# Performance work log

Measured on AMD Instinct MI355X. Metric: run time of the kernel, lower is better.

## Reference

```python
import jax, jax.numpy as jnp
import numpy as np

HEAD = 8
DIM_IN = 512
PAD = (4, 4)            # pad = head - dim % head = 8 -> (4, 4)
DIM = DIM_IN + sum(PAD) # 520
DH = DIM // HEAD        # 65


def setup_inputs() -> dict:
    key = jax.random.key(0)
    k1, k2, k3, k4 = jax.random.split(key, 4)
    B, L = 4, 2048
    inp = jax.random.normal(k1, (B, L, DIM_IN), dtype=jnp.float32)
    # nn.Linear weights, shape (out, in), bias=False
    scale = 1.0 / np.sqrt(DIM)
    w_q = jax.random.uniform(k2, (DIM, DIM), jnp.float32, -scale, scale)
    w_k = jax.random.uniform(k3, (DIM, DIM), jnp.float32, -scale, scale)
    w_v = jax.random.uniform(k4, (DIM, DIM), jnp.float32, -scale, scale)
    return {"inp": inp, "w_q": w_q, "w_k": w_k, "w_v": w_v}


def reference(inp, w_q, w_k, w_v):
    # F.pad(inp, pad) pads the last (feature) dim
    x = jnp.pad(inp, ((0, 0), (0, 0), (PAD[0], PAD[1])))
    B, L, D = x.shape
    # project then split heads: [B, H, L, dh]
    def proj(w):
        return (x @ w.T).reshape(B, L, HEAD, DH).transpose(0, 2, 1, 3)
    q, k, v = proj(w_q), proj(w_k), proj(w_v)
    score = jnp.einsum('bhqd,bhkd->bhqk', q, k) / jnp.sqrt(jnp.float32(DH))
    attn = jax.nn.softmax(score, axis=-1)          # [B, H, L, L]
    # dropout is identity in eval/reference mode
    out = jnp.einsum('bhqk,bhkd->bhqd', attn, v)
    out = out.transpose(0, 2, 1, 3).reshape(B, L, D)
    out = out[:, :, PAD[0]:-PAD[1]]                # strip feature padding
    return out, attn
```

## Files before the change

### kernel.cpp

```cpp
#include <hip/hip_runtime.h>

typedef unsigned short u16;
typedef __bf16 bf16x8 __attribute__((ext_vector_type(8)));
typedef float f32x16 __attribute__((ext_vector_type(16)));
typedef unsigned short ushort8 __attribute__((ext_vector_type(8)));

#define LOG2E 1.44269504088896340736f
#define QSCALE 0.12403473458920846f

__device__ __forceinline__ u16 f2bf(float f) {
  unsigned u = __float_as_uint(f);
  u = (u + 0x7fffu + ((u >> 16) & 1u)) >> 16;
  return (u16)u;
}

__device__ __forceinline__ f32x16 zero16() {
  f32x16 z;
#pragma unroll
  for (int i = 0; i < 16; ++i) z[i] = 0.0f;
  return z;
}

__device__ __forceinline__ void gload_lds16(const u16* g, u16* l) {
  __builtin_amdgcn_global_load_lds(
      (const __attribute__((address_space(1))) void*)g,
      (__attribute__((address_space(3))) void*)l, 16, 0, 0);
}

__global__ __launch_bounds__(256) void cvt_x_kernel(const float4* __restrict__ in,
                                                    ushort4* __restrict__ out) {
  int i = blockIdx.x * 256 + threadIdx.x;
  float4 v = in[i];
  ushort4 o;
  o.x = f2bf(v.x); o.y = f2bf(v.y); o.z = f2bf(v.z); o.w = f2bf(v.w);
  out[i] = o;
}

__global__ __launch_bounds__(256) void cvt_w_kernel(const float* __restrict__ wq,
                                                    const float* __restrict__ wk,
                                                    const float* __restrict__ wv,
                                                    u16* __restrict__ wtt) {
  int id = blockIdx.x * 256 + threadIdx.x;
  int wsel = id / (544 * 512);
  int rem = id - wsel * (544 * 512);
  int j = rem >> 9, k = rem & 511;
  const float* wp = (wsel == 0) ? wq : (wsel == 1) ? wk : wv;
  float v = (j < 520) ? wp[j * 520 + k + 4] : 0.0f;
  wtt[id] = f2bf(v);
}

__global__ __launch_bounds__(256) void zero_kernel(uint4* __restrict__ p, int n) {
  int i = blockIdx.x * 256 + threadIdx.x;
  uint4 z = make_uint4(0u, 0u, 0u, 0u);
  for (; i < n; i += gridDim.x * 256) p[i] = z;
}

__global__ __launch_bounds__(256) void proj_kernel(const u16* __restrict__ xb,
                                                   const u16* __restrict__ wtt,
                                                   u16* __restrict__ qb,
                                                   u16* __restrict__ kpl,
                                                   u16* __restrict__ vb) {
  int tid = threadIdx.x;
  int w = tid >> 6, l = tid & 63, lr = l & 31, lh = l >> 5;
  int m0 = blockIdx.y * 128 + w * 32;
  int g = blockIdx.x;

  const u16* ap = xb + (size_t)(m0 + lr) * 512 + lh * 8;

  f32x16 acc[4];
  const u16* bp[4];
  bool valid[4];
#pragma unroll
  for (int i = 0; i < 4; ++i) {
    int nt = g * 4 + i;
    valid[i] = (nt < 51);
    int ntc = valid[i] ? nt : 50;
    bp[i] = wtt + ((size_t)((ntc / 17) * 544 + (ntc % 17) * 32) + lr) * 512 + lh * 8;
    acc[i] = zero16();
  }

#pragma unroll 4
  for (int s = 0; s < 32; ++s) {
    bf16x8 a = *reinterpret_cast<const bf16x8*>(ap + s * 16);
#pragma unroll
    for (int i = 0; i < 4; ++i) {
      if (valid[i]) {
        bf16x8 b = *reinterpret_cast<const bf16x8*>(bp[i] + s * 16);
        acc[i] = __builtin_amdgcn_mfma_f32_32x32x16_bf16(a, b, acc[i], 0, 0, 0);
      }
    }
  }

#pragma unroll
  for (int i = 0; i < 4; ++i) {
    int nt = g * 4 + i;
    if (nt < 51) {
      int wsel = nt / 17;
      int j = (nt % 17) * 32 + lr;
      if (j < 520) {
        int h = j / 65, dh = j - h * 65;
#pragma unroll
        for (int r = 0; r < 16; ++r) {
          int m = m0 + (r & 3) + 8 * (r >> 2) + 4 * lh;
          int bb = m >> 11, lrow = m & 2047;
          int bh = bb * 8 + h;
          if (wsel == 0) {
            qb[((size_t)bh * 2048 + lrow) * 80 + dh] = f2bf(acc[i][r] * QSCALE);
          } else if (wsel == 1) {
            kpl[(((size_t)bh * 10 + (dh >> 3)) * 2048 + lrow) * 8 + (dh & 7)] = f2bf(acc[i][r]);
          } else {
            vb[((size_t)bh * 2048 + lrow) * 80 + dh] = f2bf(acc[i][r]);
          }
        }
      }
    }
  }
}

__global__ __launch_bounds__(256) void repack_v_kernel(const u16* __restrict__ vb,
                                                       u16* __restrict__ vpl) {
  __shared__ u16 lds[256 * 88];
  int bh = blockIdx.y;
  int key0 = blockIdx.x * 256;
  int t = threadIdx.x;

  const u16* src = vb + ((size_t)bh * 2048 + key0) * 80;
#pragma unroll
  for (int i = 0; i < 10; ++i) {
    int f16 = i * 256 + t;
    int row = f16 / 10, col = f16 % 10;
    ushort8 v = *reinterpret_cast<const ushort8*>(src + f16 * 8);
    *reinterpret_cast<ushort8*>(&lds[row * 88 + col * 8]) = v;
  }
  __syncthreads();

#pragma unroll
  for (int j = 0; j < 10; ++j) {
    int slot = j * 256 + t;
    int kc = slot / 80, d = slot - kc * 80;
    ushort8 v;
#pragma unroll
    for (int e = 0; e < 8; ++e) v[e] = lds[(kc * 8 + e) * 88 + d];
    *reinterpret_cast<ushort8*>(
        &vpl[(((size_t)bh * 256 + (key0 >> 3) + kc) * 80 + d) * 8]) = v;
  }
}

__global__ __launch_bounds__(256, 2) void attn_kernel(const u16* __restrict__ qb,
                                                      const u16* __restrict__ kpl,
                                                      const u16* __restrict__ vpl,
                                                      float* __restrict__ out,
                                                      float* __restrict__ attn) {
  __shared__ u16 kvbuf[2][10240];
  __shared__ u16 plds[4][32][40];

  int b = blockIdx.x;
  int bh = (b & 7) + 8 * (b >> 7);
  int qblk = (b >> 3) & 15;
  int tid = threadIdx.x;
  int w = tid >> 6, l = tid & 63, lr = l & 31, lh = l >> 5;
  int q0 = qblk * 128 + w * 32;
  int phase = (b * 11) & 31;

  const u16* kbh = kpl + (size_t)bh * 163840;
  const u16* vbh = vpl + (size_t)bh * 163840;

  const u16* qptr = qb + ((size_t)bh * 2048 + q0 + lr) * 80 + lh * 8;
  bf16x8 qf[5];
#pragma unroll
  for (int s = 0; s < 5; ++s) qf[s] = *reinterpret_cast<const bf16x8*>(qptr + s * 16);

  float sum[16];
#pragma unroll
  for (int r2 = 0; r2 < 16; ++r2) sum[r2] = 0.0f;

#define STAGE_K128(kt, bufi)                                                  \
  {                                                                           \
    _Pragma("unroll")                                                         \
    for (int i = 0; i < 5; ++i) {                                             \
      int idx = w + i * 4;                                                    \
      int c = idx >> 1, half = idx & 1;                                       \
      gload_lds16(kbh + (size_t)c * 16384 + (kt) * 1024 + half * 512 + l * 8, \
                  &kvbuf[bufi][idx * 512]);                                   \
    }                                                                         \
  }

  STAGE_K128(0, 0);
  __syncthreads();
  int buf = 0;
  for (int t = 0; t < 16; ++t) {
    if (t < 15) STAGE_K128(t + 1, buf ^ 1);
#pragma unroll
    for (int sub = 0; sub < 4; ++sub) {
      f32x16 acc = zero16();
#pragma unroll
      for (int s = 0; s < 5; ++s) {
        bf16x8 bk = *reinterpret_cast<const bf16x8*>(
            &kvbuf[buf][((2 * s + lh) * 128 + sub * 32 + lr) * 8]);
        acc = __builtin_amdgcn_mfma_f32_32x32x16_bf16(qf[s], bk, acc, 0, 0, 0);
      }
#pragma unroll
      for (int r2 = 0; r2 < 16; ++r2)
        sum[r2] += __builtin_amdgcn_exp2f(acc[r2] * LOG2E);
    }
    __syncthreads();
    buf ^= 1;
  }

#pragma unroll
  for (int r2 = 0; r2 < 16; ++r2) {
    float s = sum[r2];
#pragma unroll
    for (int d = 1; d < 32; d <<= 1) s += __shfl_xor(s, d);
    sum[r2] = 1.0f / s;
  }

#define STAGE_KV64(t64, bufi)                                                 \
  {                                                                           \
    _Pragma("unroll")                                                         \
    for (int i = 0; i < 5; ++i) {                                             \
      int idx = w + i * 4;                                                    \
      const u16* src = (idx < 10)                                             \
          ? kbh + (size_t)idx * 16384 + (t64) * 512 + l * 8                   \
          : vbh + (size_t)(t64) * 5120 + (idx - 10) * 512 + l * 8;            \
      gload_lds16(src, &kvbuf[bufi][idx * 512]);                              \
    }                                                                         \
  }

  f32x16 O[3];
#pragma unroll
  for (int n = 0; n < 3; ++n) O[n] = zero16();

  float* attn_base = attn + ((size_t)bh * 2048 + q0) * 2048;

  STAGE_KV64(phase, 0);
  __syncthreads();
  buf = 0;
  for (int t = 0; t < 32; ++t) {
    int tt = (t + phase) & 31;
    if (t < 31) STAGE_KV64((tt + 1) & 31, buf ^ 1);
#pragma unroll
    for (int sub = 0; sub < 2; ++sub) {
      int key0 = tt * 64 + sub * 32;
      f32x16 acc = zero16();
#pragma unroll
      for (int s = 0; s < 5; ++s) {
        bf16x8 bk = *reinterpret_cast<const bf16x8*>(
            &kvbuf[buf][((2 * s + lh) * 64 + sub * 32 + lr) * 8]);
        acc = __builtin_amdgcn_mfma_f32_32x32x16_bf16(qf[s], bk, acc, 0, 0, 0);
      }
#pragma unroll
      for (int r2 = 0; r2 < 16; ++r2) {
        int row = (r2 & 3) + 8 * (r2 >> 2) + 4 * lh;
        float p = __builtin_amdgcn_exp2f(acc[r2] * LOG2E) * sum[r2];
        __builtin_nontemporal_store(p, &attn_base[(size_t)row * 2048 + key0 + lr]);
        plds[w][row][lr] = f2bf(p);
      }
#pragma unroll
      for (int ks = 0; ks < 2; ++ks) {
        bf16x8 pa = *reinterpret_cast<const bf16x8*>(&plds[w][lr][ks * 16 + lh * 8]);
#pragma unroll
        for (int n = 0; n < 3; ++n) {
          bf16x8 bv = *reinterpret_cast<const bf16x8*>(
              &kvbuf[buf][5120 + ((sub * 4 + 2 * ks + lh) * 80 + n * 32 + lr) * 8]);
          O[n] = __builtin_amdgcn_mfma_f32_32x32x16_bf16(pa, bv, O[n], 0, 0, 0);
        }
      }
    }
    asm volatile("s_waitcnt vmcnt(32)" ::: "memory");
    __builtin_amdgcn_s_barrier();
    buf ^= 1;
  }

  int bb = bh >> 3, h = bh & 7;
#pragma unroll
  for (int n = 0; n < 3; ++n) {
    int d = n * 32 + lr;
    int cc = h * 65 + d - 4;
    if (d < 65 && cc >= 0 && cc < 512) {
#pragma unroll
      for (int r2 = 0; r2 < 16; ++r2) {
        int row = (r2 & 3) + 8 * (r2 >> 2) + 4 * lh;
        out[((size_t)bb * 2048 + q0 + row) * 512 + cc] = O[n][r2];
      }
    }
  }
}

extern "C" void kernel_launch(void* const* d_in, const int* in_sizes, int n_in,
                              void* d_out, int out_size, void* d_ws, size_t ws_size,
                              hipStream_t stream) {
  (void)in_sizes; (void)n_in; (void)out_size; (void)ws_size;
  const float* inp = (const float*)d_in[0];
  const float* wq  = (const float*)d_in[1];
  const float* wk  = (const float*)d_in[2];
  const float* wv  = (const float*)d_in[3];

  char* ws = (char*)d_ws;
  u16* xb  = (u16*)(ws + 0);
  u16* wtt = (u16*)(ws + 8388608);
  u16* qb  = (u16*)(ws + 10059776);
  u16* kpl = (u16*)(ws + 20545536);
  u16* vb  = (u16*)(ws + 31031296);
  u16* vpl = (u16*)(ws + 41517056);

  float* out  = (float*)d_out;
  float* attn = out + (size_t)4 * 2048 * 512;

  cvt_x_kernel<<<4096, 256, 0, stream>>>((const float4*)inp, (ushort4*)xb);
  cvt_w_kernel<<<3264, 256, 0, stream>>>(wq, wk, wv, wtt);
  zero_kernel<<<640, 256, 0, stream>>>((uint4*)qb, 655360);
  proj_kernel<<<dim3(13, 64), 256, 0, stream>>>(xb, wtt, qb, kpl, vb);
  repack_v_kernel<<<dim3(8, 32), 256, 0, stream>>>(vb, vpl);
  attn_kernel<<<512, 256, 0, stream>>>(qb, kpl, vpl, out, attn);
}
```

Baseline: 256.5 us.

## Transpose score MFMA so P stays in registers, vectorize attn stores

Swaps the MFMA operands so each lane holds a query column of scores. This lets the P operand for the PV MFMA be built in registers with packed bf16 conversion and permlane32 swaps instead of a bf16 LDS round trip. The row-sum reduction becomes a single cross-half shuffle. LOG2E is folded into the Q scale, and the attn tile is transposed through a small fp32 LDS buffer so it is written with 16-byte nontemporal stores instead of scalar stores. The vmcnt wait threshold is tightened, and the change relies on gfx950-specific instructions.

Measured after the change: 311.9 us. +21.6%, slower.

```diff
diff --git a/kernel.cpp b/kernel.cpp
--- a/kernel.cpp
+++ b/kernel.cpp
@@ -1,12 +1,15 @@
 #include <hip/hip_runtime.h>
 
 typedef unsigned short u16;
+typedef unsigned int u32;
 typedef __bf16 bf16x8 __attribute__((ext_vector_type(8)));
 typedef float f32x16 __attribute__((ext_vector_type(16)));
+typedef float f32x4 __attribute__((ext_vector_type(4)));
 typedef unsigned short ushort8 __attribute__((ext_vector_type(8)));
+typedef unsigned int uint4v __attribute__((ext_vector_type(4)));
 
 #define LOG2E 1.44269504088896340736f
-#define QSCALE 0.12403473458920846f
+#define QSCALE2 0.17894429680154087f
 
 __device__ __forceinline__ u16 f2bf(float f) {
   unsigned u = __float_as_uint(f);
@@ -25,6 +28,12 @@
   __builtin_amdgcn_global_load_lds(
       (const __attribute__((address_space(1))) void*)g,
       (__attribute__((address_space(3))) void*)l, 16, 0, 0);
+}
+
+__device__ __forceinline__ u32 cvtpk_bf16(float lo, float hi) {
+  u32 r;
+  asm("v_cvt_pk_bf16_f32 %0, %1, %2" : "=v"(r) : "v"(lo), "v"(hi));
+  return r;
 }
 
 __global__ __launch_bounds__(256) void cvt_x_kernel(const float4* __restrict__ in,
@@ -105,7 +114,7 @@
           int bb = m >> 11, lrow = m & 2047;
           int bh = bb * 8 + h;
           if (wsel == 0) {
-            qb[((size_t)bh * 2048 + lrow) * 80 + dh] = f2bf(acc[i][r] * QSCALE);
+            qb[((size_t)bh * 2048 + lrow) * 80 + dh] = f2bf(acc[i][r] * QSCALE2);
           } else if (wsel == 1) {
             kpl[(((size_t)bh * 10 + (dh >> 3)) * 2048 + lrow) * 8 + (dh & 7)] = f2bf(acc[i][r]);
           } else {
@@ -152,7 +161,7 @@
                                                       float* __restrict__ out,
                                                       float* __restrict__ attn) {
   __shared__ u16 kvbuf[2][10240];
-  __shared__ u16 plds[4][32][40];
+  __shared__ float stld[4][32 * 20];
 
   int b = blockIdx.x;
   int bh = (b & 7) + 8 * (b >> 7);
@@ -170,9 +179,7 @@
 #pragma unroll
   for (int s = 0; s < 5; ++s) qf[s] = *reinterpret_cast<const bf16x8*>(qptr + s * 16);
 
-  float sum[16];
-#pragma unroll
-  for (int r2 = 0; r2 < 16; ++r2) sum[r2] = 0.0f;
+  float rsum = 0.0f;
 
 #define STAGE_K128(kt, bufi)                                                  \
   {                                                                           \
@@ -197,23 +204,16 @@
       for (int s = 0; s < 5; ++s) {
         bf16x8 bk = *reinterpret_cast<const bf16x8*>(
             &kvbuf[buf][((2 * s + lh) * 128 + sub * 32 + lr) * 8]);
-        acc = __builtin_amdgcn_mfma_f32_32x32x16_bf16(qf[s], bk, acc, 0, 0, 0);
-      }
-#pragma unroll
-      for (int r2 = 0; r2 < 16; ++r2)
-        sum[r2] += __builtin_amdgcn_exp2f(acc[r2] * LOG2E);
+        acc = __builtin_amdgcn_mfma_f32_32x32x16_bf16(bk, qf[s], acc, 0, 0, 0);
+      }
+#pragma unroll
+      for (int r2 = 0; r2 < 16; ++r2) rsum += __builtin_amdgcn_exp2f(acc[r2]);
     }
     __syncthreads();
     buf ^= 1;
   }
 
-#pragma unroll
-  for (int r2 = 0; r2 < 16; ++r2) {
-    float s = sum[r2];
-#pragma unroll
-    for (int d = 1; d < 32; d <<= 1) s += __shfl_xor(s, d);
-    sum[r2] = 1.0f / s;
-  }
+  float inv = 1.0f / (rsum + __shfl_xor(rsum, 32));
 
 #define STAGE_KV64(t64, bufi)                                                 \
   {                                                                           \
@@ -232,6 +232,7 @@
   for (int n = 0; n < 3; ++n) O[n] = zero16();
 
   float* attn_base = attn + ((size_t)bh * 2048 + q0) * 2048;
+  float* srow = &stld[w][0];
 
   STAGE_KV64(phase, 0);
   __syncthreads();
@@ -247,18 +248,46 @@
       for (int s = 0; s < 5; ++s) {
         bf16x8 bk = *reinterpret_cast<const bf16x8*>(
             &kvbuf[buf][((2 * s + lh) * 64 + sub * 32 + lr) * 8]);
-        acc = __builtin_amdgcn_mfma_f32_32x32x16_bf16(qf[s], bk, acc, 0, 0, 0);
-      }
-#pragma unroll
-      for (int r2 = 0; r2 < 16; ++r2) {
-        int row = (r2 & 3) + 8 * (r2 >> 2) + 4 * lh;
-        float p = __builtin_amdgcn_exp2f(acc[r2] * LOG2E) * sum[r2];
-        __builtin_nontemporal_store(p, &attn_base[(size_t)row * 2048 + key0 + lr]);
-        plds[w][row][lr] = f2bf(p);
-      }
+        acc = __builtin_amdgcn_mfma_f32_32x32x16_bf16(bk, qf[s], acc, 0, 0, 0);
+      }
+      float p[16];
+#pragma unroll
+      for (int r2 = 0; r2 < 16; ++r2)
+        p[r2] = __builtin_amdgcn_exp2f(acc[r2]) * inv;
+
+#pragma unroll
+      for (int h = 0; h < 2; ++h) {
+#pragma unroll
+        for (int r2 = 0; r2 < 8; ++r2) {
+          int kloc = (r2 & 3) + 8 * (r2 >> 2) + 4 * lh;
+          srow[lr * 20 + kloc] = p[h * 8 + r2];
+        }
+#pragma unroll
+        for (int j = 0; j < 2; ++j) {
+          int q = j * 16 + (l >> 2);
+          f32x4 vv = *reinterpret_cast<const f32x4*>(&srow[q * 20 + (l & 3) * 4]);
+          __builtin_nontemporal_store(vv, reinterpret_cast<f32x4*>(
+              &attn_base[(size_t)q * 2048 + key0 + h * 16 + (l & 3) * 4]));
+        }
+      }
+
+      u32 u01 = cvtpk_bf16(p[0], p[1]),  u23 = cvtpk_bf16(p[2], p[3]);
+      u32 v01 = cvtpk_bf16(p[4], p[5]),  v23 = cvtpk_bf16(p[6], p[7]);
+      u32 x01 = cvtpk_bf16(p[8], p[9]),  x23 = cvtpk_bf16(p[10], p[11]);
+      u32 y01 = cvtpk_bf16(p[12], p[13]), y23 = cvtpk_bf16(p[14], p[15]);
+      asm("v_permlane32_swap_b32 %0, %1" : "+v"(u01), "+v"(v01));
+      asm("v_permlane32_swap_b32 %0, %1" : "+v"(u23), "+v"(v23));
+      asm("v_permlane32_swap_b32 %0, %1" : "+v"(x01), "+v"(y01));
+      asm("v_permlane32_swap_b32 %0, %1" : "+v"(x23), "+v"(y23));
+      uint4v pw0, pw1;
+      pw0[0] = u01; pw0[1] = u23; pw0[2] = v01; pw0[3] = v23;
+      pw1[0] = x01; pw1[1] = x23; pw1[2] = y01; pw1[3] = y23;
+      bf16x8 pa0 = __builtin_bit_cast(bf16x8, pw0);
+      bf16x8 pa1 = __builtin_bit_cast(bf16x8, pw1);
+
 #pragma unroll
       for (int ks = 0; ks < 2; ++ks) {
-        bf16x8 pa = *reinterpret_cast<const bf16x8*>(&plds[w][lr][ks * 16 + lh * 8]);
+        bf16x8 pa = ks ? pa1 : pa0;
 #pragma unroll
         for (int n = 0; n < 3; ++n) {
           bf16x8 bv = *reinterpret_cast<const bf16x8*>(
@@ -267,7 +296,7 @@
         }
       }
     }
-    asm volatile("s_waitcnt vmcnt(32)" ::: "memory");
+    asm volatile("s_waitcnt vmcnt(8)" ::: "memory");
     __builtin_amdgcn_s_barrier();
     buf ^= 1;
   }
```

## Fold log2e into Q scale and read K directly from global in sum pass

Applied to the files above, without the earlier changes.

The softmax scale and log2(e) are folded into one constant applied when Q is written, which removes a multiply per score in both passes. The first (row-sum) pass no longer stages K tiles through LDS with double buffering and barriers. Each wave now loads K fragments straight from global memory, relying on cache reuse across waves. This drops barriers and LDS traffic but adds global-load latency and depends on L1/L2 hit rates.

Measured after the change: 268.5 us. +4.7%, slower.

```diff
diff --git a/kernel.cpp b/kernel.cpp
--- a/kernel.cpp
+++ b/kernel.cpp
@@ -5,8 +5,7 @@
 typedef float f32x16 __attribute__((ext_vector_type(16)));
 typedef unsigned short ushort8 __attribute__((ext_vector_type(8)));
 
-#define LOG2E 1.44269504088896340736f
-#define QSCALE 0.12403473458920846f
+#define QSCALE2 0.17894429680154087f
 
 __device__ __forceinline__ u16 f2bf(float f) {
   unsigned u = __float_as_uint(f);
@@ -105,7 +104,7 @@
           int bb = m >> 11, lrow = m & 2047;
           int bh = bb * 8 + h;
           if (wsel == 0) {
-            qb[((size_t)bh * 2048 + lrow) * 80 + dh] = f2bf(acc[i][r] * QSCALE);
+            qb[((size_t)bh * 2048 + lrow) * 80 + dh] = f2bf(acc[i][r] * QSCALE2);
           } else if (wsel == 1) {
             kpl[(((size_t)bh * 10 + (dh >> 3)) * 2048 + lrow) * 8 + (dh & 7)] = f2bf(acc[i][r]);
           } else {
@@ -174,37 +173,18 @@
 #pragma unroll
   for (int r2 = 0; r2 < 16; ++r2) sum[r2] = 0.0f;
 
-#define STAGE_K128(kt, bufi)                                                  \
-  {                                                                           \
-    _Pragma("unroll")                                                         \
-    for (int i = 0; i < 5; ++i) {                                             \
-      int idx = w + i * 4;                                                    \
-      int c = idx >> 1, half = idx & 1;                                       \
-      gload_lds16(kbh + (size_t)c * 16384 + (kt) * 1024 + half * 512 + l * 8, \
-                  &kvbuf[bufi][idx * 512]);                                   \
-    }                                                                         \
-  }
-
-  STAGE_K128(0, 0);
-  __syncthreads();
-  int buf = 0;
-  for (int t = 0; t < 16; ++t) {
-    if (t < 15) STAGE_K128(t + 1, buf ^ 1);
-#pragma unroll
-    for (int sub = 0; sub < 4; ++sub) {
-      f32x16 acc = zero16();
-#pragma unroll
-      for (int s = 0; s < 5; ++s) {
-        bf16x8 bk = *reinterpret_cast<const bf16x8*>(
-            &kvbuf[buf][((2 * s + lh) * 128 + sub * 32 + lr) * 8]);
-        acc = __builtin_amdgcn_mfma_f32_32x32x16_bf16(qf[s], bk, acc, 0, 0, 0);
-      }
-#pragma unroll
-      for (int r2 = 0; r2 < 16; ++r2)
-        sum[r2] += __builtin_amdgcn_exp2f(acc[r2] * LOG2E);
-    }
-    __syncthreads();
-    buf ^= 1;
+  const u16* kl1 = kbh + ((size_t)lh * 2048 + lr) * 8;
+#pragma unroll 2
+  for (int t = 0; t < 64; ++t) {
+    const u16* kp = kl1 + t * 256;
+    f32x16 acc = zero16();
+#pragma unroll
+    for (int s = 0; s < 5; ++s) {
+      bf16x8 bk = *reinterpret_cast<const bf16x8*>(kp + s * 32768);
+      acc = __builtin_amdgcn_mfma_f32_32x32x16_bf16(qf[s], bk, acc, 0, 0, 0);
+    }
+#pragma unroll
+    for (int r2 = 0; r2 < 16; ++r2) sum[r2] += __builtin_amdgcn_exp2f(acc[r2]);
   }
 
 #pragma unroll
@@ -235,7 +215,7 @@
 
   STAGE_KV64(phase, 0);
   __syncthreads();
-  buf = 0;
+  int buf = 0;
   for (int t = 0; t < 32; ++t) {
     int tt = (t + phase) & 31;
     if (t < 31) STAGE_KV64((tt + 1) & 31, buf ^ 1);
@@ -252,7 +232,7 @@
 #pragma unroll
       for (int r2 = 0; r2 < 16; ++r2) {
         int row = (r2 & 3) + 8 * (r2 >> 2) + 4 * lh;
-        float p = __builtin_amdgcn_exp2f(acc[r2] * LOG2E) * sum[r2];
+        float p = __builtin_amdgcn_exp2f(acc[r2]) * sum[r2];
         __builtin_nontemporal_store(p, &attn_base[(size_t)row * 2048 + key0 + lr]);
         plds[w][row][lr] = f2bf(p);
       }
```
